# Kernel tuning notes

Hardware: AMD Instinct MI355X
Metric: run time of the kernel (lower is better)

The kernel has to match this reference:

```python
import jax, jax.numpy as jnp
import numpy as np

B = 64        # number of graph segments
BASE = 384    # mean verts per segment
LMAX = 512    # pad length (counts in [256, 512])
H_DIM = 256
H_DIV = 128   # h_dim // h_dim_div
HEADS = 4
DH = H_DIV // HEADS  # 32


def _counts(seed):
    rng = np.random.default_rng(seed)
    d = rng.integers(-128, 129, B)
    d[1::2] = -d[::2]            # paired so the total is exactly B*BASE
    return (BASE + d).astype(np.int64)


def _pad_indices(counts, L):
    # Gather indices/mask mapping packed ragged tokens -> padded [B, L].
    counts = np.asarray(counts)
    off = np.concatenate([[0], np.cumsum(counts)[:-1]])
    ar = np.arange(L)[None, :]
    mask = ar < counts[:, None]
    idx = np.where(mask, off[:, None] + ar, 0)
    return idx, mask


def setup_inputs() -> dict:
    key = jax.random.key(0)
    ks = jax.random.split(key, 16)
    src_num_verts = _counts(0)
    dst_num_verts = _counts(1)
    total = B * BASE  # 24576 for both src and dst

    def w(k, shape):
        return 0.02 * jax.random.normal(k, shape, jnp.float32)

    return {
        'src_h': jax.random.normal(ks[0], (total, H_DIM), jnp.float32),
        'dst_h': jax.random.normal(ks[1], (total, H_DIM), jnp.float32),
        'src_num_verts': src_num_verts,
        'dst_num_verts': dst_num_verts,
        # 1x1 Conv1d == linear over channels
        'Wq': w(ks[2], (H_DIV, H_DIM)), 'bq': w(ks[3], (H_DIV,)),
        'Wk': w(ks[4], (H_DIV, H_DIM)), 'bk': w(ks[5], (H_DIV,)),
        'Wv': w(ks[6], (H_DIV, H_DIM)), 'bv': w(ks[7], (H_DIV,)),
        'Wm': w(ks[8], (H_DIV, H_DIV)), 'bm': w(ks[9], (H_DIV,)),
        'W1': w(ks[10], (H_DIM, H_DIM + H_DIV)), 'b1': w(ks[11], (H_DIM,)),
        'g1': 1.0 + 0.1 * jax.random.normal(ks[12], (H_DIM,), jnp.float32),
        'be1': w(ks[13], (H_DIM,)),
        'rm1': w(ks[14], (H_DIM,)),
        'rv1': jax.random.uniform(ks[15], (H_DIM,), jnp.float32, 0.5, 1.5),
        'W2': w(jax.random.fold_in(key, 100), (H_DIM, H_DIM)),
        'b2': w(jax.random.fold_in(key, 101), (H_DIM,)),
        'g2': 1.0 + 0.1 * jax.random.normal(jax.random.fold_in(key, 102), (H_DIM,), jnp.float32),
        'be2': w(jax.random.fold_in(key, 103), (H_DIM,)),
        'rm2': w(jax.random.fold_in(key, 104), (H_DIM,)),
        'rv2': jax.random.uniform(jax.random.fold_in(key, 105), (H_DIM,), jnp.float32, 0.5, 1.5),
    }


def _bn(x, g, b, rm, rv):
    # BatchNorm1d in eval mode (running stats)
    return (x - rm) / jnp.sqrt(rv + 1e-5) * g + b


def reference(src_h, dst_h, src_num_verts, dst_num_verts,
              Wq, bq, Wk, bk, Wv, bv, Wm, bm,
              W1, b1, g1, be1, rm1, rv1,
              W2, b2, g2, be2, rm2, rv2):
    didx, dmask = _pad_indices(dst_num_verts, LMAX)
    sidx, smask = _pad_indices(src_num_verts, LMAX)

    # fused projections over all packed tokens (1x1 conv == matmul)
    q = src_h_proj = dst_h @ Wq.T + bq        # [Nd, H_DIV]
    k = src_h @ Wk.T + bk                     # [Ns, H_DIV]
    v = src_h @ Wv.T + bv

    # pad to block-diagonal batched form; channel c = d*HEADS + h per torch view
    qp = q[didx].reshape(B, LMAX, DH, HEADS)
    kp = k[sidx].reshape(B, LMAX, DH, HEADS)
    vp = v[sidx].reshape(B, LMAX, DH, HEADS)

    scores = jnp.einsum('bndh,bmdh->bhnm', qp, kp) / (DH ** 0.5)
    scores = jnp.where(jnp.asarray(smask)[:, None, None, :], scores, -1e9)
    attn = jax.nn.softmax(scores, axis=-1)
    msg = jnp.einsum('bhnm,bmdh->bndh', attn, vp).reshape(B, LMAX, H_DIV)
    msg = msg @ Wm.T + bm                     # merge conv

    bb, ii = np.nonzero(dmask)                # unpad back to packed layout
    h_msg = msg[bb, ii]                       # [Nd, H_DIV]

    x = jnp.concatenate([dst_h, h_msg], axis=-1)
    x = _bn(x @ W1.T + b1, g1, be1, rm1, rv1)
    x = jax.nn.relu(x)
    x = _bn(x @ W2.T + b2, g2, be2, rm2, rv2)
    return dst_h + x
```

## Files before the change

kernel.cpp:

```cpp
#include <hip/hip_runtime.h>
#include <hip/hip_bf16.h>
#include <math.h>

#define B_SEG 64
#define HDIM 256
#define HDIV 128
#define NHEADS 4
#define DH 32
#define QSC 0.17677669529663687f
#define QSCL 0.2550760953483594f

typedef unsigned short u16;
typedef unsigned int u32;

typedef __attribute__((ext_vector_type(8))) short s8v;
typedef __attribute__((ext_vector_type(4))) short s4v;
typedef __attribute__((ext_vector_type(4))) float f4v;

#if defined(__HIP_DEVICE_COMPILE__)
#if __has_builtin(__builtin_amdgcn_mfma_f32_16x16x16_bf16)
#define MFMA16(a, b, c) __builtin_amdgcn_mfma_f32_16x16x16_bf16(a, b, c, 0, 0, 0)
#elif __has_builtin(__builtin_amdgcn_mfma_f32_16x16x16bf16_1k)
#define MFMA16(a, b, c) __builtin_amdgcn_mfma_f32_16x16x16bf16_1k(a, b, c, 0, 0, 0)
#else
#error "no 16x16x16 bf16 mfma builtin on device"
#endif
#if __has_builtin(__builtin_amdgcn_exp2f)
#define EXP2(x) __builtin_amdgcn_exp2f(x)
#else
#define EXP2(x) exp2f(x)
#endif
#else
#define MFMA16(a, b, c) (c)
#define EXP2(x) exp2f(x)
#endif

__device__ __forceinline__ u16 f2bf(float f) {
    u32 v;
    __builtin_memcpy(&v, &f, 4);
    u32 r = v + 0x7fffu + ((v >> 16) & 1u);
    return (u16)(r >> 16);
}

__device__ __forceinline__ void async_cp16(const u16* g, u16* l) {
    __builtin_amdgcn_global_load_lds(
        (const __attribute__((address_space(1))) u32*)g,
        (__attribute__((address_space(3))) u32*)l, 16, 0, 0);
}

__global__ __launch_bounds__(256) void k_prep(
    const float* __restrict__ Wq, const float* __restrict__ bq,
    const float* __restrict__ Wk, const float* __restrict__ bk,
    const float* __restrict__ Wv, const float* __restrict__ bv,
    const float* __restrict__ Wm, const float* __restrict__ bm,
    const float* __restrict__ W1, const float* __restrict__ b1,
    const float* __restrict__ g1, const float* __restrict__ be1,
    const float* __restrict__ rm1, const float* __restrict__ rv1,
    const float* __restrict__ W2, const float* __restrict__ b2,
    const float* __restrict__ g2, const float* __restrict__ be2,
    const float* __restrict__ rm2, const float* __restrict__ rv2,
    const int* __restrict__ sc_raw, const int* __restrict__ dc_raw,
    const float* __restrict__ src_h, const float* __restrict__ dst_h,
    int* __restrict__ meta,
    u16* __restrict__ pWq, u16* __restrict__ pWkv,
    u16* __restrict__ pW1f, u16* __restrict__ pW2,
    float* __restrict__ bqp, float* __restrict__ bkvp,
    float* __restrict__ sc1, float* __restrict__ sh1,
    float* __restrict__ sc2, float* __restrict__ sh2,
    u16* __restrict__ srcb, u16* __restrict__ dstb, int ntot) {
    if (blockIdx.x < 1028) {
        int idx = blockIdx.x * 256 + threadIdx.x;
        if (idx < 32768) {
            int cp = idx >> 8, k = idx & 255;
            int c = ((cp & 31) << 2) | (cp >> 5);
            pWq[idx] = f2bf(Wq[c * 256 + k]);
        } else if (idx < 98304) {
            int i = idx - 32768;
            int rp = i >> 8, k = i & 255;
            int r = rp & 127;
            int c = ((r & 31) << 2) | (r >> 5);
            float v = (rp < 128) ? Wk[c * 256 + k] : Wv[c * 256 + k];
            pWkv[i] = f2bf(v);
        } else if (idx < 163840) {
            int i = idx - 98304;
            int o = i >> 8, k = i & 255;
            pW1f[o * 384 + k] = f2bf(W1[o * 384 + k]);
        } else if (idx < 196608) {
            int i = idx - 163840;
            int o = i >> 7, cp = i & 127;
            int c = ((cp & 31) << 2) | (cp >> 5);
            float acc = 0.f;
            for (int j = 0; j < 128; j++)
                acc += W1[o * 384 + 256 + j] * Wm[j * 128 + c];
            pW1f[o * 384 + 256 + cp] = f2bf(acc);
        } else if (idx < 262144) {
            int i = idx - 196608;
            pW2[i] = f2bf(W2[i]);
        } else if (idx < 263168) {
            int p = idx - 262144;
            if (p < 128) {
                int c = ((p & 31) << 2) | (p >> 5);
                bqp[p] = bq[c] * QSCL;
            } else if (p < 384) {
                int r = p - 128; int rr = r & 127;
                int c = ((rr & 31) << 2) | (rr >> 5);
                bkvp[r] = (r < 128) ? bk[c] : bv[c];
            } else if (p < 640) {
                int o = p - 384;
                float bsum = 0.f;
                for (int j = 0; j < 128; j++)
                    bsum += W1[o * 384 + 256 + j] * bm[j];
                float s = g1[o] * rsqrtf(rv1[o] + 1e-5f);
                sc1[o] = s;
                sh1[o] = (b1[o] + bsum - rm1[o]) * s + be1[o];
            } else if (p < 896) {
                int o = p - 640;
                float s = g2[o] * rsqrtf(rv2[o] + 1e-5f);
                sc2[o] = s;
                sh2[o] = (b2[o] - rm2[o]) * s + be2[o];
            }
        }
    } else if (blockIdx.x == 1028) {
        if (threadIdx.x == 0) {
            bool is64 = (sc_raw[1] == 0);
            int so = 0, dofs = 0;
            for (int i = 0; i < B_SEG; i++) {
                int s = is64 ? sc_raw[2 * i] : sc_raw[i];
                int d = is64 ? dc_raw[2 * i] : dc_raw[i];
                meta[i] = s; meta[64 + i] = d;
                meta[128 + i] = so; meta[192 + i] = dofs;
                so += s; dofs += d;
            }
        }
    } else {
        int i = (blockIdx.x - 1029) * 256 + threadIdx.x;
        int half = ntot * 64;
        const float4* s;
        u16* o;
        int j = i;
        if (i < half) { s = (const float4*)src_h; o = srcb; }
        else { s = (const float4*)dst_h; o = dstb; j = i - half; }
        float4 v = s[j];
        ushort4 u = {f2bf(v.x), f2bf(v.y), f2bf(v.z), f2bf(v.w)};
        ((ushort4*)o)[j] = u;
    }
}

__device__ __forceinline__ void q_body(
    const u16* __restrict__ A, const u16* __restrict__ Bw,
    const float* __restrict__ shift, u16* __restrict__ Cout, int m0,
    u16* Al, u16* Bl) {
    int tid = threadIdx.x;
    int w = tid >> 6, lane = tid & 63;
    int wm = w & 1, wn = w >> 1;
    int l15 = lane & 15, quad = lane >> 4;
    int srow = w * 16 + (lane >> 2);
    int scol = (lane & 3) << 3;
    f4v acc[4][2] = {};

    auto STAGE = [&](int buf, int k0) {
        u16* al0 = Al + buf * 4096 + w * 512;
        u16* bl0 = Bl + buf * 4096 + w * 512;
        async_cp16(&A[(size_t)(m0 + srow) * 256 + k0 + scol], al0);
        async_cp16(&Bw[(size_t)srow * 256 + k0 + scol], bl0);
    };

    STAGE(0, 0);
    __syncthreads();
    int cur = 0;
    for (int k0 = 0; k0 < 256; k0 += 32) {
        if (k0 + 32 < 256) STAGE(cur ^ 1, k0 + 32);
        const u16* Ab = Al + cur * 4096;
        const u16* Bb = Bl + cur * 4096;
        s8v af[4], bf[2];
#pragma unroll
        for (int i = 0; i < 4; i++)
            af[i] = *(const s8v*)(&Ab[(wm * 64 + i * 16 + l15) * 32 + quad * 8]);
#pragma unroll
        for (int j = 0; j < 2; j++)
            bf[j] = *(const s8v*)(&Bb[(wn * 32 + j * 16 + l15) * 32 + quad * 8]);
#pragma unroll
        for (int i = 0; i < 4; i++)
#pragma unroll
            for (int j = 0; j < 2; j++)
                acc[i][j] = __builtin_amdgcn_mfma_f32_16x16x32_bf16(
                    af[i], bf[j], acc[i][j], 0, 0, 0);
        __syncthreads();
        cur ^= 1;
    }
#pragma unroll
    for (int i = 0; i < 4; i++) {
#pragma unroll
        for (int j = 0; j < 2; j++) {
            int n = wn * 32 + j * 16 + l15;
            float sh = shift[n];
#pragma unroll
            for (int r = 0; r < 4; r++) {
                int m = m0 + wm * 64 + i * 16 + quad * 4 + r;
                Cout[(size_t)m * 128 + n] = f2bf(acc[i][j][r] + sh);
            }
        }
    }
}

__device__ __forceinline__ void kv_body(
    const u16* __restrict__ A, const u16* __restrict__ Bw,
    const float* __restrict__ shift, u16* __restrict__ Cout, int m0,
    u16* Al, u16* Bl) {
    int tid = threadIdx.x;
    int w = tid >> 6, lane = tid & 63;
    int wm = w & 1, wn = w >> 1;
    int l15 = lane & 15, quad = lane >> 4;
    int srowA = w * 16 + (lane >> 2);
    int srowB = w * 32 + (lane >> 2);
    int scol = (lane & 3) << 3;
    f4v acc[4][4] = {};

    auto STAGE = [&](int buf, int k0) {
        u16* al0 = Al + buf * 4096 + w * 512;
        u16* bl0 = Bl + buf * 8192 + w * 1024;
        async_cp16(&A[(size_t)(m0 + srowA) * 256 + k0 + scol], al0);
        async_cp16(&Bw[(size_t)srowB * 256 + k0 + scol], bl0);
        async_cp16(&Bw[(size_t)(srowB + 16) * 256 + k0 + scol], bl0 + 512);
    };

    STAGE(0, 0);
    __syncthreads();
    int cur = 0;
    for (int k0 = 0; k0 < 256; k0 += 32) {
        if (k0 + 32 < 256) STAGE(cur ^ 1, k0 + 32);
        const u16* Ab = Al + cur * 4096;
        const u16* Bb = Bl + cur * 8192;
        s8v af[4];
#pragma unroll
        for (int i = 0; i < 4; i++)
            af[i] = *(const s8v*)(&Ab[(wm * 64 + i * 16 + l15) * 32 + quad * 8]);
#pragma unroll
        for (int j = 0; j < 4; j++) {
            s8v bf = *(const s8v*)(&Bb[(wn * 64 + j * 16 + l15) * 32 + quad * 8]);
#pragma unroll
            for (int i = 0; i < 4; i++)
                acc[i][j] = __builtin_amdgcn_mfma_f32_16x16x32_bf16(
                    af[i], bf, acc[i][j], 0, 0, 0);
        }
        __syncthreads();
        cur ^= 1;
    }
#pragma unroll
    for (int i = 0; i < 4; i++) {
#pragma unroll
        for (int j = 0; j < 4; j++) {
            int n = wn * 64 + j * 16 + l15;
            float sh = shift[n];
#pragma unroll
            for (int r = 0; r < 4; r++) {
                int m = m0 + wm * 64 + i * 16 + quad * 4 + r;
                Cout[(size_t)m * 256 + n] = f2bf(acc[i][j][r] + sh);
            }
        }
    }
}

__global__ __launch_bounds__(512, 4) void k_qkv(
    const u16* __restrict__ dstb, const u16* __restrict__ srcb,
    const u16* __restrict__ pWq, const u16* __restrict__ pWkv,
    const float* __restrict__ bqp, const float* __restrict__ bkvp,
    u16* __restrict__ qb, u16* __restrict__ kvb) {
    __shared__ u16 Al[8192];
    __shared__ u16 Bl[16384];
    int m0 = blockIdx.x * 128;
    if (blockIdx.y == 0)
        q_body(dstb, pWq, bqp, qb, m0, Al, Bl);
    else
        kv_body(srcb, pWkv, bkvp, kvb, m0, Al, Bl);
}

__global__ __launch_bounds__(256, 4) void k_mlp(
    const u16* __restrict__ dstb, const u16* __restrict__ msgb,
    const u16* __restrict__ pW1f, const u16* __restrict__ pW2,
    const float* __restrict__ sc1, const float* __restrict__ sh1,
    const float* __restrict__ sc2, const float* __restrict__ sh2,
    const float* __restrict__ dst_h, float* __restrict__ out) {
    __shared__ u16 Al[2048];
    __shared__ u16 Bl[16384];
    __shared__ u16 X1[32 * 256];
    int m0 = blockIdx.x * 32;
    int tid = threadIdx.x;
    int w = tid >> 6, lane = tid & 63;
    int l15 = lane & 15, quad = lane >> 4;
    int srow = lane >> 2;
    int scol = (lane & 3) << 3;
    f4v acc[2][4];

    auto STAGE1 = [&](int buf, int k0) {
        const u16* Ag; int aL, acol;
        if (k0 < 256) { Ag = dstb; aL = 256; acol = k0; }
        else { Ag = msgb; aL = 128; acol = k0 - 256; }
#pragma unroll
        for (int q = 0; q < 4; q++)
            async_cp16(&pW1f[(size_t)(w * 64 + q * 16 + srow) * 384 + k0 + scol],
                       Bl + buf * 8192 + (w * 64 + q * 16) * 32);
        if (w < 2)
            async_cp16(&Ag[(size_t)(m0 + w * 16 + srow) * aL + acol + scol],
                       Al + buf * 1024 + w * 16 * 32);
    };
    auto STAGE2 = [&](int buf, int k0) {
#pragma unroll
        for (int q = 0; q < 4; q++)
            async_cp16(&pW2[(size_t)(w * 64 + q * 16 + srow) * 256 + k0 + scol],
                       Bl + buf * 8192 + (w * 64 + q * 16) * 32);
    };

#pragma unroll
    for (int i = 0; i < 2; i++)
#pragma unroll
        for (int j = 0; j < 4; j++) acc[i][j] = (f4v){0.f, 0.f, 0.f, 0.f};

    STAGE1(0, 0);
    __syncthreads();
    int cur = 0;
    for (int k0 = 0; k0 < 384; k0 += 32) {
        if (k0 + 32 < 384) STAGE1(cur ^ 1, k0 + 32);
        const u16* Ab = Al + cur * 1024;
        const u16* Bb = Bl + cur * 8192;
        s8v af[2], bf[4];
#pragma unroll
        for (int i = 0; i < 2; i++)
            af[i] = *(const s8v*)(&Ab[(i * 16 + l15) * 32 + quad * 8]);
#pragma unroll
        for (int j = 0; j < 4; j++)
            bf[j] = *(const s8v*)(&Bb[(w * 64 + j * 16 + l15) * 32 + quad * 8]);
#pragma unroll
        for (int i = 0; i < 2; i++)
#pragma unroll
            for (int j = 0; j < 4; j++)
                acc[i][j] = __builtin_amdgcn_mfma_f32_16x16x32_bf16(
                    af[i], bf[j], acc[i][j], 0, 0, 0);
        __syncthreads();
        cur ^= 1;
    }

    STAGE2(0, 0);
#pragma unroll
    for (int i = 0; i < 2; i++) {
#pragma unroll
        for (int j = 0; j < 4; j++) {
            int n = w * 64 + j * 16 + l15;
            float sc = sc1[n], sh = sh1[n];
#pragma unroll
            for (int r = 0; r < 4; r++) {
                int row = i * 16 + quad * 4 + r;
                float v = fmaxf(acc[i][j][r] * sc + sh, 0.f);
                X1[row * 256 + ((n >> 3) ^ (row & 7)) * 8 + (n & 7)] = f2bf(v);
            }
        }
    }
    __syncthreads();

#pragma unroll
    for (int i = 0; i < 2; i++)
#pragma unroll
        for (int j = 0; j < 4; j++) acc[i][j] = (f4v){0.f, 0.f, 0.f, 0.f};

    cur = 0;
    for (int k0 = 0; k0 < 256; k0 += 32) {
        if (k0 + 32 < 256) STAGE2(cur ^ 1, k0 + 32);
        const u16* Bb = Bl + cur * 8192;
        s8v af[2], bf[4];
#pragma unroll
        for (int i = 0; i < 2; i++) {
            int row = i * 16 + l15;
            af[i] = *(const s8v*)(
                &X1[row * 256 + (((k0 >> 3) + quad) ^ (row & 7)) * 8]);
        }
#pragma unroll
        for (int j = 0; j < 4; j++)
            bf[j] = *(const s8v*)(&Bb[(w * 64 + j * 16 + l15) * 32 + quad * 8]);
#pragma unroll
        for (int i = 0; i < 2; i++)
#pragma unroll
            for (int j = 0; j < 4; j++)
                acc[i][j] = __builtin_amdgcn_mfma_f32_16x16x32_bf16(
                    af[i], bf[j], acc[i][j], 0, 0, 0);
        __syncthreads();
        cur ^= 1;
    }
#pragma unroll
    for (int i = 0; i < 2; i++) {
#pragma unroll
        for (int j = 0; j < 4; j++) {
            int n = w * 64 + j * 16 + l15;
            float sc = sc2[n], sh = sh2[n];
#pragma unroll
            for (int r = 0; r < 4; r++) {
                int m = m0 + i * 16 + quad * 4 + r;
                float v = acc[i][j][r] * sc + sh + dst_h[(size_t)m * 256 + n];
                out[(size_t)m * 256 + n] = v;
            }
        }
    }
}

__global__ __launch_bounds__(512, 4) void k_attn(
    const u16* __restrict__ qb, const u16* __restrict__ kvb,
    const int* __restrict__ meta, u16* __restrict__ msgb) {
    extern __shared__ u16 sm[];
    u16* Kl = sm;
    u16* Vl = sm + 16384;
    int b = blockIdx.x, h = blockIdx.y, z = blockIdx.z;
    int ns = meta[b], nd = meta[64 + b];
    int soff = meta[128 + b], doff = meta[192 + b];
    int tid = threadIdx.x, w = tid >> 6, lane = tid & 63;
    int l15 = lane & 15, quad = lane >> 4;

    {
        int m = tid;
        if (m < ns) {
            const uint4* ks = (const uint4*)&kvb[(size_t)(soff + m) * 256 + h * 32];
#pragma unroll
            for (int s = 0; s < 4; s++)
                *(uint4*)&Kl[m * 32 + (s ^ ((m >> 1) & 3)) * 8] = ks[s];
            uint4 vv[4];
            const uint4* vs =
                (const uint4*)&kvb[(size_t)(soff + m) * 256 + 128 + h * 32];
#pragma unroll
            for (int s = 0; s < 4; s++) vv[s] = vs[s];
            const u16* pv = (const u16*)vv;
#pragma unroll
            for (int d = 0; d < 32; d++)
                Vl[d * 512 + ((m >> 3) ^ (d & 7)) * 8 + (m & 7)] = pv[d];
        } else {
#pragma unroll
            for (int d = 0; d < 32; d++)
                Vl[d * 512 + ((m >> 3) ^ (d & 7)) * 8 + (m & 7)] = 0;
        }
    }
    __syncthreads();

    int nfull = ns >> 5;
    int nc32 = (ns + 31) >> 5;
    int ksw = (quad ^ ((l15 >> 1) & 3)) * 8;
    int vsw = l15 & 7;
    int half4 = (quad & 1) * 4;
    const u16* VlLo = Vl + l15 * 512;
    const u16* VlHi = Vl + (16 + l15) * 512;

    for (int s0 = (z * 8 + w) * 16; s0 < nd; s0 += 256) {
        int qr = min(s0 + l15, nd - 1);
        s8v aq = *(const s8v*)&qb[(size_t)(doff + qr) * 128 + h * 32 + quad * 8];

        f4v oa0 = {0.f, 0.f, 0.f, 0.f};
        f4v oa1 = {0.f, 0.f, 0.f, 0.f};
        float lsum = 0.f;
        for (int c = 0; c < nc32; c++) {
            int kr0 = c * 32 + l15;
            s8v bk0 = *(const s8v*)&Kl[kr0 * 32 + ksw];
            s8v bk1 = *(const s8v*)&Kl[(kr0 + 16) * 32 + ksw];
            f4v sa = __builtin_amdgcn_mfma_f32_16x16x32_bf16(
                bk0, aq, (f4v){0.f, 0.f, 0.f, 0.f}, 0, 0, 0);
            f4v sb = __builtin_amdgcn_mfma_f32_16x16x32_bf16(
                bk1, aq, (f4v){0.f, 0.f, 0.f, 0.f}, 0, 0, 0);
            float e0[4], e1[4];
            if (c < nfull) {
#pragma unroll
                for (int r = 0; r < 4; r++) {
                    float va = EXP2(sa[r]);
                    float vb = EXP2(sb[r]);
                    e0[r] = va; e1[r] = vb;
                    lsum += va + vb;
                }
            } else {
                int kb = c * 32 + quad * 4;
#pragma unroll
                for (int r = 0; r < 4; r++) {
                    float va = (kb + r < ns) ? EXP2(sa[r]) : 0.f;
                    float vb = (kb + 16 + r < ns) ? EXP2(sb[r]) : 0.f;
                    e0[r] = va; e1[r] = vb;
                    lsum += va + vb;
                }
            }
            union { s4v v; u32 u[2]; } pb0, pb1;
            pb0.u[0] = (u32)f2bf(e0[0]) | ((u32)f2bf(e0[1]) << 16);
            pb0.u[1] = (u32)f2bf(e0[2]) | ((u32)f2bf(e0[3]) << 16);
            pb1.u[0] = (u32)f2bf(e1[0]) | ((u32)f2bf(e1[1]) << 16);
            pb1.u[1] = (u32)f2bf(e1[2]) | ((u32)f2bf(e1[3]) << 16);
            int slb = c * 4 + (quad >> 1);
            s4v v00 = *(const s4v*)&VlLo[(slb ^ vsw) * 8 + half4];
            s4v v01 = *(const s4v*)&VlLo[((slb + 2) ^ vsw) * 8 + half4];
            s4v v10 = *(const s4v*)&VlHi[(slb ^ vsw) * 8 + half4];
            s4v v11 = *(const s4v*)&VlHi[((slb + 2) ^ vsw) * 8 + half4];
            oa0 = MFMA16(v00, pb0.v, oa0);
            oa0 = MFMA16(v01, pb1.v, oa0);
            oa1 = MFMA16(v10, pb0.v, oa1);
            oa1 = MFMA16(v11, pb1.v, oa1);
        }
        lsum += __shfl_xor(lsum, 16, 64);
        lsum += __shfl_xor(lsum, 32, 64);
        float inv = 1.f / lsum;
        int row = s0 + l15;
        if (row < nd) {
            size_t base = (size_t)(doff + row) * 128 + h * 32;
            ushort4 o0 = {f2bf(oa0[0] * inv), f2bf(oa0[1] * inv),
                          f2bf(oa0[2] * inv), f2bf(oa0[3] * inv)};
            ushort4 o1 = {f2bf(oa1[0] * inv), f2bf(oa1[1] * inv),
                          f2bf(oa1[2] * inv), f2bf(oa1[3] * inv)};
            *(ushort4*)&msgb[base + quad * 4] = o0;
            *(ushort4*)&msgb[base + 16 + quad * 4] = o1;
        }
    }
}

extern "C" void kernel_launch(void* const* d_in, const int* in_sizes, int n_in,
                              void* d_out, int out_size, void* d_ws, size_t ws_size,
                              hipStream_t stream) {
    const float* src_h = (const float*)d_in[0];
    const float* dst_h = (const float*)d_in[1];
    const int* snv = (const int*)d_in[2];
    const int* dnv = (const int*)d_in[3];
    const float* Wq = (const float*)d_in[4];  const float* bq = (const float*)d_in[5];
    const float* Wk = (const float*)d_in[6];  const float* bk = (const float*)d_in[7];
    const float* Wv = (const float*)d_in[8];  const float* bv = (const float*)d_in[9];
    const float* Wm = (const float*)d_in[10]; const float* bm = (const float*)d_in[11];
    const float* W1 = (const float*)d_in[12]; const float* b1 = (const float*)d_in[13];
    const float* g1 = (const float*)d_in[14]; const float* be1 = (const float*)d_in[15];
    const float* rm1 = (const float*)d_in[16]; const float* rv1 = (const float*)d_in[17];
    const float* W2 = (const float*)d_in[18]; const float* b2 = (const float*)d_in[19];
    const float* g2 = (const float*)d_in[20]; const float* be2 = (const float*)d_in[21];
    const float* rm2 = (const float*)d_in[22]; const float* rv2 = (const float*)d_in[23];

    int ntot = out_size / HDIM;
    int mt = ntot / 128;

    char* ws = (char*)d_ws;
    int* meta = (int*)ws;
    float* bqp = (float*)(ws + 4096);
    float* bkvp = (float*)(ws + 4608);
    float* sc1 = (float*)(ws + 6144);
    float* sh1 = (float*)(ws + 7168);
    float* sc2 = (float*)(ws + 8192);
    float* sh2 = (float*)(ws + 9216);
    u16* pWq = (u16*)(ws + 16384);
    u16* pWkv = (u16*)(ws + 81920);
    u16* pW1f = (u16*)(ws + 212992);
    u16* pW2 = (u16*)(ws + 409600);
    u16* srcb = (u16*)(ws + 1048576);
    u16* dstb = (u16*)(ws + 13631488);
    u16* msgb = (u16*)(ws + 26214400);

    u16* qb = (u16*)d_out;
    u16* kvb = qb + (size_t)ntot * 128;

    (void)hipFuncSetAttribute((const void*)k_attn,
                              hipFuncAttributeMaxDynamicSharedMemorySize, 65536);

    k_prep<<<dim3(1029 + ntot / 2), dim3(256), 0, stream>>>(
        Wq, bq, Wk, bk, Wv, bv, Wm, bm, W1, b1, g1, be1, rm1, rv1,
        W2, b2, g2, be2, rm2, rv2, snv, dnv, src_h, dst_h, meta,
        pWq, pWkv, pW1f, pW2, bqp, bkvp, sc1, sh1, sc2, sh2,
        srcb, dstb, ntot);
    k_qkv<<<dim3(mt, 2), dim3(512), 0, stream>>>(
        dstb, srcb, pWq, pWkv, bqp, bkvp, qb, kvb);
    k_attn<<<dim3(B_SEG, NHEADS, 2), dim3(512), 65536, stream>>>(
        qb, kvb, meta, msgb);
    k_mlp<<<dim3(ntot / 32), dim3(256), 0, stream>>>(
        dstb, msgb, pW1f, pW2, sc1, sh1, sc2, sh2, dst_h, (float*)d_out);
}
```

Measured before the change: 200.2 us.

## Fuse fp32-to-bf16 input conversion into QKV GEMM loads

The projection kernels now stage fp32 src_h and dst_h rows directly into LDS, using an XOR swizzle to avoid bank conflicts, and convert them to bf16 in registers before the MFMA. This drops the separate conversion pass in k_prep and the bf16 src copy. The dst bf16 copy that k_mlp still needs is produced by a third grid slice of k_qkv. This saves a full read and write pass over the inputs, at the cost of twice the LDS for the A tiles (occupancy hint lowered to 2) and conversion ALU work inside the GEMM loop.

```diff
diff --git a/kernel.cpp b/kernel.cpp
--- a/kernel.cpp
+++ b/kernel.cpp
@@ -42,6 +42,15 @@
     return (u16)(r >> 16);
 }
 
+__device__ __forceinline__ uint4 cvt8(float4 a, float4 b) {
+    uint4 r;
+    r.x = ((u32)f2bf(a.y) << 16) | f2bf(a.x);
+    r.y = ((u32)f2bf(a.w) << 16) | f2bf(a.z);
+    r.z = ((u32)f2bf(b.y) << 16) | f2bf(b.x);
+    r.w = ((u32)f2bf(b.w) << 16) | f2bf(b.z);
+    return r;
+}
+
 __device__ __forceinline__ void async_cp16(const u16* g, u16* l) {
     __builtin_amdgcn_global_load_lds(
         (const __attribute__((address_space(1))) u32*)g,
@@ -60,14 +69,12 @@
     const float* __restrict__ g2, const float* __restrict__ be2,
     const float* __restrict__ rm2, const float* __restrict__ rv2,
     const int* __restrict__ sc_raw, const int* __restrict__ dc_raw,
-    const float* __restrict__ src_h, const float* __restrict__ dst_h,
     int* __restrict__ meta,
     u16* __restrict__ pWq, u16* __restrict__ pWkv,
     u16* __restrict__ pW1f, u16* __restrict__ pW2,
     float* __restrict__ bqp, float* __restrict__ bkvp,
     float* __restrict__ sc1, float* __restrict__ sh1,
-    float* __restrict__ sc2, float* __restrict__ sh2,
-    u16* __restrict__ srcb, u16* __restrict__ dstb, int ntot) {
+    float* __restrict__ sc2, float* __restrict__ sh2) {
     if (blockIdx.x < 1028) {
         int idx = blockIdx.x * 256 + threadIdx.x;
         if (idx < 32768) {
@@ -120,7 +127,7 @@
                 sh2[o] = (b2[o] - rm2[o]) * s + be2[o];
             }
         }
-    } else if (blockIdx.x == 1028) {
+    } else {
         if (threadIdx.x == 0) {
             bool is64 = (sc_raw[1] == 0);
             int so = 0, dofs = 0;
@@ -132,37 +139,31 @@
                 so += s; dofs += d;
             }
         }
-    } else {
-        int i = (blockIdx.x - 1029) * 256 + threadIdx.x;
-        int half = ntot * 64;
-        const float4* s;
-        u16* o;
-        int j = i;
-        if (i < half) { s = (const float4*)src_h; o = srcb; }
-        else { s = (const float4*)dst_h; o = dstb; j = i - half; }
-        float4 v = s[j];
-        ushort4 u = {f2bf(v.x), f2bf(v.y), f2bf(v.z), f2bf(v.w)};
-        ((ushort4*)o)[j] = u;
     }
 }
 
 __device__ __forceinline__ void q_body(
-    const u16* __restrict__ A, const u16* __restrict__ Bw,
+    const float* __restrict__ A, const u16* __restrict__ Bw,
     const float* __restrict__ shift, u16* __restrict__ Cout, int m0,
-    u16* Al, u16* Bl) {
+    float* Af, u16* Bl) {
     int tid = threadIdx.x;
     int w = tid >> 6, lane = tid & 63;
     int wm = w & 1, wn = w >> 1;
     int l15 = lane & 15, quad = lane >> 4;
-    int srow = w * 16 + (lane >> 2);
-    int scol = (lane & 3) << 3;
+    int sr8 = lane >> 3;
     f4v acc[4][2] = {};
 
     auto STAGE = [&](int buf, int k0) {
-        u16* al0 = Al + buf * 4096 + w * 512;
-        u16* bl0 = Bl + buf * 4096 + w * 512;
-        async_cp16(&A[(size_t)(m0 + srow) * 256 + k0 + scol], al0);
-        async_cp16(&Bw[(size_t)srow * 256 + k0 + scol], bl0);
+#pragma unroll
+        for (int j = 0; j < 2; j++) {
+            int row = w * 16 + j * 8 + sr8;
+            int gs = (lane & 7) ^ (row & 7);
+            async_cp16((const u16*)&A[(size_t)(m0 + row) * 256 + k0 + gs * 4],
+                       (u16*)(Af + buf * 4096 + w * 512 + j * 256));
+        }
+        async_cp16(&Bw[(size_t)(w * 16 + (lane >> 2)) * 256 + k0 +
+                       ((lane & 3) << 3)],
+                   Bl + buf * 4096 + w * 512);
     };
 
     STAGE(0, 0);
@@ -170,12 +171,18 @@
     int cur = 0;
     for (int k0 = 0; k0 < 256; k0 += 32) {
         if (k0 + 32 < 256) STAGE(cur ^ 1, k0 + 32);
-        const u16* Ab = Al + cur * 4096;
+        const float* Ab = Af + cur * 4096;
         const u16* Bb = Bl + cur * 4096;
         s8v af[4], bf[2];
 #pragma unroll
-        for (int i = 0; i < 4; i++)
-            af[i] = *(const s8v*)(&Ab[(wm * 64 + i * 16 + l15) * 32 + quad * 8]);
+        for (int i = 0; i < 4; i++) {
+            int rA = wm * 64 + i * 16 + l15;
+            float4 a0 = *(const float4*)&Ab[rA * 32 + (((2 * quad) ^ (rA & 7)) << 2)];
+            float4 a1 = *(const float4*)&Ab[rA * 32 + (((2 * quad + 1) ^ (rA & 7)) << 2)];
+            union { uint4 u; s8v v; } cv;
+            cv.u = cvt8(a0, a1);
+            af[i] = cv.v;
+        }
 #pragma unroll
         for (int j = 0; j < 2; j++)
             bf[j] = *(const s8v*)(&Bb[(wn * 32 + j * 16 + l15) * 32 + quad * 8]);
@@ -204,22 +211,27 @@
 }
 
 __device__ __forceinline__ void kv_body(
-    const u16* __restrict__ A, const u16* __restrict__ Bw,
+    const float* __restrict__ A, const u16* __restrict__ Bw,
     const float* __restrict__ shift, u16* __restrict__ Cout, int m0,
-    u16* Al, u16* Bl) {
+    float* Af, u16* Bl) {
     int tid = threadIdx.x;
     int w = tid >> 6, lane = tid & 63;
     int wm = w & 1, wn = w >> 1;
     int l15 = lane & 15, quad = lane >> 4;
-    int srowA = w * 16 + (lane >> 2);
+    int sr8 = lane >> 3;
     int srowB = w * 32 + (lane >> 2);
     int scol = (lane & 3) << 3;
     f4v acc[4][4] = {};
 
     auto STAGE = [&](int buf, int k0) {
-        u16* al0 = Al + buf * 4096 + w * 512;
+#pragma unroll
+        for (int j = 0; j < 2; j++) {
+            int row = w * 16 + j * 8 + sr8;
+            int gs = (lane & 7) ^ (row & 7);
+            async_cp16((const u16*)&A[(size_t)(m0 + row) * 256 + k0 + gs * 4],
+                       (u16*)(Af + buf * 4096 + w * 512 + j * 256));
+        }
         u16* bl0 = Bl + buf * 8192 + w * 1024;
-        async_cp16(&A[(size_t)(m0 + srowA) * 256 + k0 + scol], al0);
         async_cp16(&Bw[(size_t)srowB * 256 + k0 + scol], bl0);
         async_cp16(&Bw[(size_t)(srowB + 16) * 256 + k0 + scol], bl0 + 512);
     };
@@ -229,12 +241,18 @@
     int cur = 0;
     for (int k0 = 0; k0 < 256; k0 += 32) {
         if (k0 + 32 < 256) STAGE(cur ^ 1, k0 + 32);
-        const u16* Ab = Al + cur * 4096;
+        const float* Ab = Af + cur * 4096;
         const u16* Bb = Bl + cur * 8192;
         s8v af[4];
 #pragma unroll
-        for (int i = 0; i < 4; i++)
-            af[i] = *(const s8v*)(&Ab[(wm * 64 + i * 16 + l15) * 32 + quad * 8]);
+        for (int i = 0; i < 4; i++) {
+            int rA = wm * 64 + i * 16 + l15;
+            float4 a0 = *(const float4*)&Ab[rA * 32 + (((2 * quad) ^ (rA & 7)) << 2)];
+            float4 a1 = *(const float4*)&Ab[rA * 32 + (((2 * quad + 1) ^ (rA & 7)) << 2)];
+            union { uint4 u; s8v v; } cv;
+            cv.u = cvt8(a0, a1);
+            af[i] = cv.v;
+        }
 #pragma unroll
         for (int j = 0; j < 4; j++) {
             s8v bf = *(const s8v*)(&Bb[(wn * 64 + j * 16 + l15) * 32 + quad * 8]);
@@ -261,18 +279,30 @@
     }
 }
 
-__global__ __launch_bounds__(512, 4) void k_qkv(
-    const u16* __restrict__ dstb, const u16* __restrict__ srcb,
+__global__ __launch_bounds__(512, 2) void k_qkv(
+    const float* __restrict__ dst_h, const float* __restrict__ src_h,
     const u16* __restrict__ pWq, const u16* __restrict__ pWkv,
     const float* __restrict__ bqp, const float* __restrict__ bkvp,
-    u16* __restrict__ qb, u16* __restrict__ kvb) {
-    __shared__ u16 Al[8192];
+    u16* __restrict__ qb, u16* __restrict__ kvb, u16* __restrict__ dstb) {
+    __shared__ float Af[8192];
     __shared__ u16 Bl[16384];
     int m0 = blockIdx.x * 128;
     if (blockIdx.y == 0)
-        q_body(dstb, pWq, bqp, qb, m0, Al, Bl);
-    else
-        kv_body(srcb, pWkv, bkvp, kvb, m0, Al, Bl);
+        q_body(dst_h, pWq, bqp, qb, m0, Af, Bl);
+    else if (blockIdx.y == 1)
+        kv_body(src_h, pWkv, bkvp, kvb, m0, Af, Bl);
+    else {
+        int t = blockIdx.x * 512 + threadIdx.x;
+        const float4* s = (const float4*)dst_h;
+        ushort4* o4 = (ushort4*)dstb;
+#pragma unroll
+        for (int i = 0; i < 16; i++) {
+            int j = t + i * 98304;
+            float4 v = s[j];
+            ushort4 u = {f2bf(v.x), f2bf(v.y), f2bf(v.z), f2bf(v.w)};
+            o4[j] = u;
+        }
+    }
 }
 
 __global__ __launch_bounds__(256, 4) void k_mlp(
@@ -543,7 +573,6 @@
     u16* pWkv = (u16*)(ws + 81920);
     u16* pW1f = (u16*)(ws + 212992);
     u16* pW2 = (u16*)(ws + 409600);
-    u16* srcb = (u16*)(ws + 1048576);
     u16* dstb = (u16*)(ws + 13631488);
     u16* msgb = (u16*)(ws + 26214400);
 
@@ -553,13 +582,12 @@
     (void)hipFuncSetAttribute((const void*)k_attn,
                               hipFuncAttributeMaxDynamicSharedMemorySize, 65536);
 
-    k_prep<<<dim3(1029 + ntot / 2), dim3(256), 0, stream>>>(
+    k_prep<<<dim3(1029), dim3(256), 0, stream>>>(
         Wq, bq, Wk, bk, Wv, bv, Wm, bm, W1, b1, g1, be1, rm1, rv1,
-        W2, b2, g2, be2, rm2, rv2, snv, dnv, src_h, dst_h, meta,
-        pWq, pWkv, pW1f, pW2, bqp, bkvp, sc1, sh1, sc2, sh2,
-        srcb, dstb, ntot);
-    k_qkv<<<dim3(mt, 2), dim3(512), 0, stream>>>(
-        dstb, srcb, pWq, pWkv, bqp, bkvp, qb, kvb);
+        W2, b2, g2, be2, rm2, rv2, snv, dnv, meta,
+        pWq, pWkv, pW1f, pW2, bqp, bkvp, sc1, sh1, sc2, sh2);
+    k_qkv<<<dim3(mt, 3), dim3(512), 0, stream>>>(
+        dst_h, src_h, pWq, pWkv, bqp, bkvp, qb, kvb, dstb);
     k_attn<<<dim3(B_SEG, NHEADS, 2), dim3(512), 65536, stream>>>(
         qb, kvb, meta, msgb);
     k_mlp<<<dim3(ntot / 32), dim3(256), 0, stream>>>(
```

Result: slower. 211.1 us (+5.4%).
